# Optimization experiments

Measured on AMD Instinct MI355X. Metric: run time of the kernel, lower is better.

Reference implementation:

```python
import jax, jax.numpy as jnp
import numpy as np

N_NODES = 10000
N_EDGES = 320000
HIDDEN = 256
HEADS = 8
HEAD_DIM = HIDDEN // HEADS  # 32
NEG_SLOPE = 0.2


def setup_inputs() -> dict:
    key = jax.random.key(0)
    ks = jax.random.split(key, 12)
    x = jax.random.normal(ks[0], (N_NODES, HIDDEN), dtype=jnp.float32)
    edges_idx = jax.random.randint(ks[1], (2, N_EDGES), 0, N_NODES, dtype=jnp.int64)
    s = 1.0 / np.sqrt(HIDDEN)
    # layer 1 params
    W1 = jax.random.normal(ks[2], (HIDDEN, HEADS * HEAD_DIM), dtype=jnp.float32) * s
    a_src1 = jax.random.normal(ks[3], (HEADS, HEAD_DIM), dtype=jnp.float32) * s
    a_dst1 = jax.random.normal(ks[4], (HEADS, HEAD_DIM), dtype=jnp.float32) * s
    b1 = jnp.zeros((HEADS * HEAD_DIM,), dtype=jnp.float32)
    # layer 2 params
    W2 = jax.random.normal(ks[5], (HIDDEN, HEADS * HEAD_DIM), dtype=jnp.float32) * s
    a_src2 = jax.random.normal(ks[6], (HEADS, HEAD_DIM), dtype=jnp.float32) * s
    a_dst2 = jax.random.normal(ks[7], (HEADS, HEAD_DIM), dtype=jnp.float32) * s
    b2 = jnp.zeros((HEADS * HEAD_DIM,), dtype=jnp.float32)
    return {"x": x, "edges_idx": edges_idx,
            "W1": W1, "a_src1": a_src1, "a_dst1": a_dst1, "b1": b1,
            "W2": W2, "a_src2": a_src2, "a_dst2": a_dst2, "b2": b2}


def gat_conv(x, src, dst, W, a_src, a_dst, b):
    """PyG GATConv (concat=True, negative_slope=0.2), dropout in eval mode."""
    N = x.shape[0]
    h = (x @ W).reshape(N, HEADS, HEAD_DIM)          # [N,H,C]
    alpha_s = jnp.einsum('nhc,hc->nh', h, a_src)     # [N,H]
    alpha_d = jnp.einsum('nhc,hc->nh', h, a_dst)     # [N,H]
    e = alpha_s[src] + alpha_d[dst]                  # [E,H]
    e = jnp.where(e > 0, e, NEG_SLOPE * e)           # leaky_relu
    # scatter-softmax over incoming edges of each dst node
    m = jax.ops.segment_max(e, dst, num_segments=N)  # [N,H]
    ex = jnp.exp(e - m[dst])                         # [E,H]
    denom = jax.ops.segment_sum(ex, dst, num_segments=N)  # [N,H]
    alpha = ex / (denom[dst] + 1e-16)                # [E,H]
    msg = h[src] * alpha[:, :, None]                 # [E,H,C]
    out = jax.ops.segment_sum(msg, dst, num_segments=N)   # [N,H,C]
    return out.reshape(N, HEADS * HEAD_DIM) + b


def reference(x, edges_idx, W1, a_src1, a_dst1, b1, W2, a_src2, a_dst2, b2):
    src = edges_idx[0]
    dst = edges_idx[1]
    h = gat_conv(x, src, dst, W1, a_src1, a_dst1, b1)
    h = jax.nn.elu(h)
    out = gat_conv(h, src, dst, W2, a_src2, a_dst2, b2)
    return out
```

## Files before the change

### kernel.cpp

```cpp
#include <hip/hip_runtime.h>
#include <hip/hip_bf16.h>
#include <hip/hip_fp16.h>

#define N_NODES 10000
#define N_EDGES 320000
#define HIDDEN 256
#define HEADS 8
#define HEAD_DIM 32
#define NEG_SLOPE 0.2f
#define CAP 80

typedef __attribute__((ext_vector_type(8))) short short8;
typedef __attribute__((ext_vector_type(8))) _Float16 half8;
typedef __attribute__((ext_vector_type(4))) float f32x4;

__device__ __forceinline__ void bf16_split(float v, unsigned short& hi, unsigned short& lo) {
    __hip_bfloat16 hb = __float2bfloat16(v);
    float hf = __bfloat162float(hb);
    __hip_bfloat16 lb = __float2bfloat16(v - hf);
    hi = *reinterpret_cast<unsigned short*>(&hb);
    lo = *reinterpret_cast<unsigned short*>(&lb);
}

__global__ __launch_bounds__(256) void prep_kernel(
    const float* __restrict__ W1, const float* __restrict__ W2,
    const int* __restrict__ src, const int* __restrict__ dst,
    unsigned short* __restrict__ w1h, unsigned short* __restrict__ w1l,
    unsigned short* __restrict__ w2h, unsigned short* __restrict__ w2l,
    int* __restrict__ counts, int* __restrict__ csr_src) {
    int b = blockIdx.x;
    int tid = threadIdx.x;
    if (b < 512) {
        int i = b * 256 + tid;
        int which = i >> 16;
        int rem = i & 0xFFFF;
        int k = rem >> 8, n = rem & 255;
        const float* W = which ? W2 : W1;
        unsigned short* wh = which ? w2h : w1h;
        unsigned short* wl = which ? w2l : w1l;
        unsigned short h, l;
        bf16_split(W[k * 256 + n], h, l);
        wh[n * 256 + k] = h;
        wl[n * 256 + k] = l;
    } else {
        int e = (b - 512) * 256 + tid;
        int d = dst[e];
        int rank = atomicAdd(&counts[d], 1);
        csr_src[d * CAP + rank] = src[e];
    }
}

template <int AFP32>
__global__ __launch_bounds__(256) void gemm_mfma_kernel(
    const float* __restrict__ Axf,
    const unsigned short* __restrict__ Ah, const unsigned short* __restrict__ Al,
    const unsigned short* __restrict__ BhT, const unsigned short* __restrict__ BlT,
    _Float16* __restrict__ hH, const float* __restrict__ a_src,
    const float* __restrict__ a_dst, float* __restrict__ alpha_s,
    float* __restrict__ alpha_d) {
    __shared__ __align__(16) unsigned short sAh[80 * 40];
    __shared__ __align__(16) unsigned short sAl[80 * 40];
    __shared__ __align__(16) unsigned short sBh[128 * 40];
    __shared__ __align__(16) unsigned short sBl[128 * 40];
    __shared__ __align__(16) _Float16 sOut[80 * 264];
    const int tid = threadIdx.x;
    const int w = tid >> 6, lane = tid & 63;
    const int col = lane & 15, quad = lane >> 4;
    const int m0 = blockIdx.y * 80, n0 = blockIdx.x * 128;

    f32x4 acc[5][2] = {};

    float4 raf[3];
    uint4 rau[3];
    uint4 rb[4];

#define LOAD_A(k0)                                                              \
    if (AFP32) {                                                                \
        _Pragma("unroll") for (int i = 0; i < 3; ++i) {                         \
            int t = tid + i * 256;                                              \
            if (t < 640) {                                                      \
                int row = t >> 3, seg = t & 7;                                  \
                raf[i] = *(const float4*)&Axf[(size_t)(m0 + row) * 256 + (k0) + seg * 4]; \
            }                                                                   \
        }                                                                       \
    } else {                                                                    \
        _Pragma("unroll") for (int i = 0; i < 3; ++i) {                         \
            int t = tid + i * 256;                                              \
            if (t < 640) {                                                      \
                int tt = t < 320 ? t : t - 320;                                 \
                int row = tt >> 2, seg = tt & 3;                                \
                const unsigned short* P = t < 320 ? Ah : Al;                    \
                rau[i] = *(const uint4*)&P[(size_t)(m0 + row) * 256 + (k0) + seg * 8]; \
            }                                                                   \
        }                                                                       \
    }
#define LOAD_B(k0)                                                              \
    _Pragma("unroll") for (int i = 0; i < 4; ++i) {                             \
        int t = tid + i * 256;                                                  \
        int tt = t < 512 ? t : t - 512;                                         \
        int row = tt >> 2, seg = tt & 3;                                        \
        const unsigned short* P = t < 512 ? BhT : BlT;                          \
        rb[i] = *(const uint4*)&P[(size_t)(n0 + row) * 256 + (k0) + seg * 8];   \
    }

    LOAD_A(0)
    LOAD_B(0)

    for (int ks = 0; ks < 8; ++ks) {
        if (AFP32) {
#pragma unroll
            for (int i = 0; i < 3; ++i) {
                int t = tid + i * 256;
                if (t < 640) {
                    int row = t >> 3, seg = t & 7;
                    float4 v = raf[i];
                    ushort4 hh, ll;
                    unsigned short hb, lb;
                    bf16_split(v.x, hb, lb); hh.x = hb; ll.x = lb;
                    bf16_split(v.y, hb, lb); hh.y = hb; ll.y = lb;
                    bf16_split(v.z, hb, lb); hh.z = hb; ll.z = lb;
                    bf16_split(v.w, hb, lb); hh.w = hb; ll.w = lb;
                    *(ushort4*)&sAh[row * 40 + seg * 4] = hh;
                    *(ushort4*)&sAl[row * 40 + seg * 4] = ll;
                }
            }
        } else {
#pragma unroll
            for (int i = 0; i < 3; ++i) {
                int t = tid + i * 256;
                if (t < 640) {
                    int tt = t < 320 ? t : t - 320;
                    int row = tt >> 2, seg = tt & 3;
                    unsigned short* S = t < 320 ? sAh : sAl;
                    *(uint4*)&S[row * 40 + seg * 8] = rau[i];
                }
            }
        }
#pragma unroll
        for (int i = 0; i < 4; ++i) {
            int t = tid + i * 256;
            int tt = t < 512 ? t : t - 512;
            int row = tt >> 2, seg = tt & 3;
            unsigned short* S = t < 512 ? sBh : sBl;
            *(uint4*)&S[row * 40 + seg * 8] = rb[i];
        }
        __syncthreads();

        if (ks < 7) {
            int nk = (ks + 1) * 32;
            LOAD_A(nk)
            LOAD_B(nk)
        }

        short8 bh0 = *(const short8*)&sBh[(w * 32 + col) * 40 + quad * 8];
        short8 bl0 = *(const short8*)&sBl[(w * 32 + col) * 40 + quad * 8];
        short8 bh1 = *(const short8*)&sBh[(w * 32 + 16 + col) * 40 + quad * 8];
        short8 bl1 = *(const short8*)&sBl[(w * 32 + 16 + col) * 40 + quad * 8];
#pragma unroll
        for (int rt = 0; rt < 5; ++rt) {
            short8 ah = *(const short8*)&sAh[(rt * 16 + col) * 40 + quad * 8];
            short8 al = *(const short8*)&sAl[(rt * 16 + col) * 40 + quad * 8];
            acc[rt][0] = __builtin_amdgcn_mfma_f32_16x16x32_bf16(ah, bh0, acc[rt][0], 0, 0, 0);
            acc[rt][0] = __builtin_amdgcn_mfma_f32_16x16x32_bf16(ah, bl0, acc[rt][0], 0, 0, 0);
            acc[rt][0] = __builtin_amdgcn_mfma_f32_16x16x32_bf16(al, bh0, acc[rt][0], 0, 0, 0);
            acc[rt][1] = __builtin_amdgcn_mfma_f32_16x16x32_bf16(ah, bh1, acc[rt][1], 0, 0, 0);
            acc[rt][1] = __builtin_amdgcn_mfma_f32_16x16x32_bf16(ah, bl1, acc[rt][1], 0, 0, 0);
            acc[rt][1] = __builtin_amdgcn_mfma_f32_16x16x32_bf16(al, bh1, acc[rt][1], 0, 0, 0);
        }
        __syncthreads();
    }
#undef LOAD_A
#undef LOAD_B

    const int head = blockIdx.x * 4 + w;
    float as0 = a_src[n0 + w * 32 + col];
    float as1 = a_src[n0 + w * 32 + 16 + col];
    float ad0 = a_dst[n0 + w * 32 + col];
    float ad1 = a_dst[n0 + w * 32 + 16 + col];
#pragma unroll
    for (int rt = 0; rt < 5; ++rt) {
#pragma unroll
        for (int r = 0; r < 4; ++r) {
            int row = rt * 16 + quad * 4 + r;
            sOut[row * 264 + w * 32 + col]      = (_Float16)acc[rt][0][r];
            sOut[row * 264 + w * 32 + 16 + col] = (_Float16)acc[rt][1][r];
            float ps = acc[rt][0][r] * as0 + acc[rt][1][r] * as1;
            float pd = acc[rt][0][r] * ad0 + acc[rt][1][r] * ad1;
#pragma unroll
            for (int m = 1; m < 16; m <<= 1) {
                ps += __shfl_xor(ps, m);
                pd += __shfl_xor(pd, m);
            }
            if (col == 0) {
                int gm = m0 + row;
                alpha_s[gm * HEADS + head] = ps;
                alpha_d[gm * HEADS + head] = pd;
            }
        }
    }
    __syncthreads();
#pragma unroll
    for (int i = 0; i < 5; ++i) {
        int t = tid + i * 256;
        int row = t >> 4, seg = t & 15;
        *(half8*)&hH[(size_t)(m0 + row) * 256 + n0 + seg * 8] =
            *(const half8*)&sOut[row * 264 + seg * 8];
    }
}

__global__ __launch_bounds__(256) void aggregate_kernel(
    const int* __restrict__ counts, const int* __restrict__ csr_src,
    const float* __restrict__ alpha_s, const float* __restrict__ alpha_d,
    const _Float16* __restrict__ hH, const float* __restrict__ bias,
    float* __restrict__ outf, unsigned short* __restrict__ oh,
    unsigned short* __restrict__ ol, int mode) {
    const int tid = threadIdx.x;
    const int w = tid >> 6, lane = tid & 63;
    const int ph = blockIdx.x / 2500;
    const int d = (blockIdx.x - ph * 2500) * 4 + w;
    const int q = lane >> 4, fl = lane & 15;
    const int hd = ph * 4 + (fl >> 2);
    const float ad = alpha_d[d * HEADS + hd];
    const int n = counts[d];
    const int* __restrict__ bucket = csr_src + d * CAP;

    const _Float16* hp = hH + ph * 128 + fl * 8;
    float acc[8] = {};
    float den = 0.f;

    int i = q * 4;
    for (; i + 3 < n; i += 16) {
        int4 s4 = *(const int4*)&bucket[i];
        float al0 = alpha_s[s4.x * HEADS + hd];
        float al1 = alpha_s[s4.y * HEADS + hd];
        float al2 = alpha_s[s4.z * HEADS + hd];
        float al3 = alpha_s[s4.w * HEADS + hd];
        half8 h0 = *(const half8*)&hp[(size_t)s4.x * HIDDEN];
        half8 h1 = *(const half8*)&hp[(size_t)s4.y * HIDDEN];
        half8 h2 = *(const half8*)&hp[(size_t)s4.z * HIDDEN];
        half8 h3 = *(const half8*)&hp[(size_t)s4.w * HIDDEN];
        float e0 = al0 + ad; e0 = e0 > 0.f ? e0 : NEG_SLOPE * e0;
        float e1 = al1 + ad; e1 = e1 > 0.f ? e1 : NEG_SLOPE * e1;
        float e2 = al2 + ad; e2 = e2 > 0.f ? e2 : NEG_SLOPE * e2;
        float e3 = al3 + ad; e3 = e3 > 0.f ? e3 : NEG_SLOPE * e3;
        float ev0 = __expf(e0), ev1 = __expf(e1);
        float ev2 = __expf(e2), ev3 = __expf(e3);
        den += (ev0 + ev1) + (ev2 + ev3);
#pragma unroll
        for (int j = 0; j < 8; ++j)
            acc[j] += (float)h0[j] * ev0 + (float)h1[j] * ev1 +
                      (float)h2[j] * ev2 + (float)h3[j] * ev3;
    }
    for (; i < n; ++i) {
        int s0 = bucket[i];
        float al0 = alpha_s[s0 * HEADS + hd];
        half8 h0 = *(const half8*)&hp[(size_t)s0 * HIDDEN];
        float e0 = al0 + ad; e0 = e0 > 0.f ? e0 : NEG_SLOPE * e0;
        float ev0 = __expf(e0);
        den += ev0;
#pragma unroll
        for (int j = 0; j < 8; ++j) acc[j] += (float)h0[j] * ev0;
    }

#pragma unroll
    for (int j = 0; j < 8; ++j) acc[j] += __shfl_xor(acc[j], 16);
    den += __shfl_xor(den, 16);
#pragma unroll
    for (int j = 0; j < 8; ++j) acc[j] += __shfl_xor(acc[j], 32);
    den += __shfl_xor(den, 32);

    if (q == 0) {
        float inv = 1.f / (den + 1e-16f);
        float v[8];
#pragma unroll
        for (int j = 0; j < 8; ++j)
            v[j] = acc[j] * inv + bias[ph * 128 + fl * 8 + j];
        size_t oidx = (size_t)d * HIDDEN + ph * 128 + fl * 8;
        if (mode == 1) {
            unsigned short hb[8], lb[8];
#pragma unroll
            for (int j = 0; j < 8; ++j) {
                v[j] = v[j] > 0.f ? v[j] : (__expf(v[j]) - 1.f);
                bf16_split(v[j], hb[j], lb[j]);
            }
            *(ushort4*)&oh[oidx]     = make_ushort4(hb[0], hb[1], hb[2], hb[3]);
            *(ushort4*)&oh[oidx + 4] = make_ushort4(hb[4], hb[5], hb[6], hb[7]);
            *(ushort4*)&ol[oidx]     = make_ushort4(lb[0], lb[1], lb[2], lb[3]);
            *(ushort4*)&ol[oidx + 4] = make_ushort4(lb[4], lb[5], lb[6], lb[7]);
        } else {
            *(float4*)&outf[oidx]     = make_float4(v[0], v[1], v[2], v[3]);
            *(float4*)&outf[oidx + 4] = make_float4(v[4], v[5], v[6], v[7]);
        }
    }
}

extern "C" void kernel_launch(void* const* d_in, const int* in_sizes, int n_in,
                              void* d_out, int out_size, void* d_ws, size_t ws_size,
                              hipStream_t stream) {
    const float* x      = (const float*)d_in[0];
    const int*   edges  = (const int*)d_in[1];
    const float* W1     = (const float*)d_in[2];
    const float* as1    = (const float*)d_in[3];
    const float* ad1    = (const float*)d_in[4];
    const float* b1     = (const float*)d_in[5];
    const float* W2     = (const float*)d_in[6];
    const float* as2    = (const float*)d_in[7];
    const float* ad2    = (const float*)d_in[8];
    const float* b2     = (const float*)d_in[9];
    float* out = (float*)d_out;

    const int* src = edges;
    const int* dst = edges + N_EDGES;

    const size_t NF = (size_t)N_NODES * HIDDEN;
    const size_t NH = (size_t)N_NODES * HEADS;

    char* base = (char*)d_ws;
    _Float16* hH = (_Float16*)base;             base += NF * 2;
    unsigned short* x2h = (unsigned short*)base; base += NF * 2;
    unsigned short* x2l = (unsigned short*)base; base += NF * 2;
    float* alpha_s = (float*)base;              base += NH * 4;
    float* alpha_d = (float*)base;              base += NH * 4;
    unsigned short* w1h = (unsigned short*)base; base += 65536 * 2;
    unsigned short* w1l = (unsigned short*)base; base += 65536 * 2;
    unsigned short* w2h = (unsigned short*)base; base += 65536 * 2;
    unsigned short* w2l = (unsigned short*)base; base += 65536 * 2;
    int* csr_src = (int*)base;                  base += (size_t)N_NODES * CAP * 4;
    int* counts  = (int*)base;                  base += (size_t)N_NODES * 4;

    dim3 gemm_grid(2, 125);
    const int EB = (N_EDGES + 255) / 256;
    const int AGG_B = 2500 * 2;

    hipMemsetAsync(counts, 0, N_NODES * sizeof(int), stream);
    prep_kernel<<<512 + EB, 256, 0, stream>>>(W1, W2, src, dst,
                                              w1h, w1l, w2h, w2l, counts, csr_src);

    gemm_mfma_kernel<1><<<gemm_grid, 256, 0, stream>>>(
        x, nullptr, nullptr, w1h, w1l, hH, as1, ad1, alpha_s, alpha_d);
    aggregate_kernel<<<AGG_B, 256, 0, stream>>>(counts, csr_src, alpha_s, alpha_d,
                                                hH, b1, nullptr, x2h, x2l, 1);

    gemm_mfma_kernel<0><<<gemm_grid, 256, 0, stream>>>(
        nullptr, x2h, x2l, w2h, w2l, hH, as2, ad2, alpha_s, alpha_d);
    aggregate_kernel<<<AGG_B, 256, 0, stream>>>(counts, csr_src, alpha_s, alpha_d,
                                                hH, b2, out, nullptr, nullptr, 0);
}
```

Baseline: 195.6 us.

## Double-buffer GEMM register prefetch and software-pipeline aggregate gathers

The GEMM kernel now holds two register stages of A/B tiles, so global loads are issued two k-steps ahead of their use rather than one. The aggregate kernel drops the variable-trip loop for a fully unrolled sequence of up to five 16-edge chunks, each with clamped indices and masked exponents, so the next chunk's gathers are issued before the current chunk is computed. Both changes aim to hide global memory latency with more loads in flight. The cost is higher register pressure, which can lower occupancy, and the aggregate path is limited to at most 80 edges per node (CAP).

```diff
diff --git a/kernel.cpp b/kernel.cpp
--- a/kernel.cpp
+++ b/kernel.cpp
@@ -70,17 +70,17 @@
 
     f32x4 acc[5][2] = {};
 
-    float4 raf[3];
-    uint4 rau[3];
-    uint4 rb[4];
-
-#define LOAD_A(k0)                                                              \
+    float4 raf[2][3];
+    uint4 rau[2][3];
+    uint4 rb[2][4];
+
+#define LOAD_A(k0, SS)                                                          \
     if (AFP32) {                                                                \
         _Pragma("unroll") for (int i = 0; i < 3; ++i) {                         \
             int t = tid + i * 256;                                              \
             if (t < 640) {                                                      \
                 int row = t >> 3, seg = t & 7;                                  \
-                raf[i] = *(const float4*)&Axf[(size_t)(m0 + row) * 256 + (k0) + seg * 4]; \
+                raf[SS][i] = *(const float4*)&Axf[(size_t)(m0 + row) * 256 + (k0) + seg * 4]; \
             }                                                                   \
         }                                                                       \
     } else {                                                                    \
@@ -90,66 +90,69 @@
                 int tt = t < 320 ? t : t - 320;                                 \
                 int row = tt >> 2, seg = tt & 3;                                \
                 const unsigned short* P = t < 320 ? Ah : Al;                    \
-                rau[i] = *(const uint4*)&P[(size_t)(m0 + row) * 256 + (k0) + seg * 8]; \
+                rau[SS][i] = *(const uint4*)&P[(size_t)(m0 + row) * 256 + (k0) + seg * 8]; \
             }                                                                   \
         }                                                                       \
     }
-#define LOAD_B(k0)                                                              \
+#define LOAD_B(k0, SS)                                                          \
     _Pragma("unroll") for (int i = 0; i < 4; ++i) {                             \
         int t = tid + i * 256;                                                  \
         int tt = t < 512 ? t : t - 512;                                         \
         int row = tt >> 2, seg = tt & 3;                                        \
         const unsigned short* P = t < 512 ? BhT : BlT;                          \
-        rb[i] = *(const uint4*)&P[(size_t)(n0 + row) * 256 + (k0) + seg * 8];   \
-    }
-
-    LOAD_A(0)
-    LOAD_B(0)
-
+        rb[SS][i] = *(const uint4*)&P[(size_t)(n0 + row) * 256 + (k0) + seg * 8]; \
+    }
+#define WRITE_A(SS)                                                             \
+    if (AFP32) {                                                                \
+        _Pragma("unroll") for (int i = 0; i < 3; ++i) {                         \
+            int t = tid + i * 256;                                              \
+            if (t < 640) {                                                      \
+                int row = t >> 3, seg = t & 7;                                  \
+                float4 v = raf[SS][i];                                          \
+                ushort4 hh, ll;                                                 \
+                unsigned short hb, lb;                                          \
+                bf16_split(v.x, hb, lb); hh.x = hb; ll.x = lb;                  \
+                bf16_split(v.y, hb, lb); hh.y = hb; ll.y = lb;                  \
+                bf16_split(v.z, hb, lb); hh.z = hb; ll.z = lb;                  \
+                bf16_split(v.w, hb, lb); hh.w = hb; ll.w = lb;                  \
+                *(ushort4*)&sAh[row * 40 + seg * 4] = hh;                       \
+                *(ushort4*)&sAl[row * 40 + seg * 4] = ll;                       \
+            }                                                                   \
+        }                                                                       \
+    } else {                                                                    \
+        _Pragma("unroll") for (int i = 0; i < 3; ++i) {                         \
+            int t = tid + i * 256;                                              \
+            if (t < 640) {                                                      \
+                int tt = t < 320 ? t : t - 320;                                 \
+                int row = tt >> 2, seg = tt & 3;                                \
+                unsigned short* Sp = t < 320 ? sAh : sAl;                       \
+                *(uint4*)&Sp[row * 40 + seg * 8] = rau[SS][i];                  \
+            }                                                                   \
+        }                                                                       \
+    }
+#define WRITE_B(SS)                                                             \
+    _Pragma("unroll") for (int i = 0; i < 4; ++i) {                             \
+        int t = tid + i * 256;                                                  \
+        int tt = t < 512 ? t : t - 512;                                         \
+        int row = tt >> 2, seg = tt & 3;                                        \
+        unsigned short* Sp = t < 512 ? sBh : sBl;                               \
+        *(uint4*)&Sp[row * 40 + seg * 8] = rb[SS][i];                           \
+    }
+
+    LOAD_A(0, 0)
+    LOAD_B(0, 0)
+    LOAD_A(32, 1)
+    LOAD_B(32, 1)
+
+#pragma unroll
     for (int ks = 0; ks < 8; ++ks) {
-        if (AFP32) {
-#pragma unroll
-            for (int i = 0; i < 3; ++i) {
-                int t = tid + i * 256;
-                if (t < 640) {
-                    int row = t >> 3, seg = t & 7;
-                    float4 v = raf[i];
-                    ushort4 hh, ll;
-                    unsigned short hb, lb;
-                    bf16_split(v.x, hb, lb); hh.x = hb; ll.x = lb;
-                    bf16_split(v.y, hb, lb); hh.y = hb; ll.y = lb;
-                    bf16_split(v.z, hb, lb); hh.z = hb; ll.z = lb;
-                    bf16_split(v.w, hb, lb); hh.w = hb; ll.w = lb;
-                    *(ushort4*)&sAh[row * 40 + seg * 4] = hh;
-                    *(ushort4*)&sAl[row * 40 + seg * 4] = ll;
-                }
-            }
-        } else {
-#pragma unroll
-            for (int i = 0; i < 3; ++i) {
-                int t = tid + i * 256;
-                if (t < 640) {
-                    int tt = t < 320 ? t : t - 320;
-                    int row = tt >> 2, seg = tt & 3;
-                    unsigned short* S = t < 320 ? sAh : sAl;
-                    *(uint4*)&S[row * 40 + seg * 8] = rau[i];
-                }
-            }
-        }
-#pragma unroll
-        for (int i = 0; i < 4; ++i) {
-            int t = tid + i * 256;
-            int tt = t < 512 ? t : t - 512;
-            int row = tt >> 2, seg = tt & 3;
-            unsigned short* S = t < 512 ? sBh : sBl;
-            *(uint4*)&S[row * 40 + seg * 8] = rb[i];
-        }
+        WRITE_A(ks & 1)
+        WRITE_B(ks & 1)
         __syncthreads();
 
-        if (ks < 7) {
-            int nk = (ks + 1) * 32;
-            LOAD_A(nk)
-            LOAD_B(nk)
+        if (ks < 6) {
+            LOAD_A((ks + 2) * 32, ks & 1)
+            LOAD_B((ks + 2) * 32, ks & 1)
         }
 
         short8 bh0 = *(const short8*)&sBh[(w * 32 + col) * 40 + quad * 8];
@@ -171,6 +174,8 @@
     }
 #undef LOAD_A
 #undef LOAD_B
+#undef WRITE_A
+#undef WRITE_B
 
     const int head = blockIdx.x * 4 + w;
     float as0 = a_src[n0 + w * 32 + col];
@@ -223,44 +228,71 @@
     const float ad = alpha_d[d * HEADS + hd];
     const int n = counts[d];
     const int* __restrict__ bucket = csr_src + d * CAP;
+    const int qb = q * 4;
 
     const _Float16* hp = hH + ph * 128 + fl * 8;
     float acc[8] = {};
     float den = 0.f;
 
-    int i = q * 4;
-    for (; i + 3 < n; i += 16) {
-        int4 s4 = *(const int4*)&bucket[i];
-        float al0 = alpha_s[s4.x * HEADS + hd];
-        float al1 = alpha_s[s4.y * HEADS + hd];
-        float al2 = alpha_s[s4.z * HEADS + hd];
-        float al3 = alpha_s[s4.w * HEADS + hd];
-        half8 h0 = *(const half8*)&hp[(size_t)s4.x * HIDDEN];
-        half8 h1 = *(const half8*)&hp[(size_t)s4.y * HIDDEN];
-        half8 h2 = *(const half8*)&hp[(size_t)s4.z * HIDDEN];
-        half8 h3 = *(const half8*)&hp[(size_t)s4.w * HIDDEN];
-        float e0 = al0 + ad; e0 = e0 > 0.f ? e0 : NEG_SLOPE * e0;
-        float e1 = al1 + ad; e1 = e1 > 0.f ? e1 : NEG_SLOPE * e1;
-        float e2 = al2 + ad; e2 = e2 > 0.f ? e2 : NEG_SLOPE * e2;
-        float e3 = al3 + ad; e3 = e3 > 0.f ? e3 : NEG_SLOPE * e3;
-        float ev0 = __expf(e0), ev1 = __expf(e1);
-        float ev2 = __expf(e2), ev3 = __expf(e3);
-        den += (ev0 + ev1) + (ev2 + ev3);
-#pragma unroll
-        for (int j = 0; j < 8; ++j)
-            acc[j] += (float)h0[j] * ev0 + (float)h1[j] * ev1 +
-                      (float)h2[j] * ev2 + (float)h3[j] * ev3;
-    }
-    for (; i < n; ++i) {
-        int s0 = bucket[i];
-        float al0 = alpha_s[s0 * HEADS + hd];
-        half8 h0 = *(const half8*)&hp[(size_t)s0 * HIDDEN];
-        float e0 = al0 + ad; e0 = e0 > 0.f ? e0 : NEG_SLOPE * e0;
-        float ev0 = __expf(e0);
-        den += ev0;
-#pragma unroll
-        for (int j = 0; j < 8; ++j) acc[j] += (float)h0[j] * ev0;
-    }
+    int4 s0_ = make_int4(0, 0, 0, 0), s1_ = s0_, s2_ = s0_, s3_ = s0_, s4_ = s0_;
+    if (n > 0)  s0_ = *(const int4*)&bucket[qb];
+    if (n > 16) s1_ = *(const int4*)&bucket[qb + 16];
+    if (n > 32) s2_ = *(const int4*)&bucket[qb + 32];
+    if (n > 48) s3_ = *(const int4*)&bucket[qb + 48];
+    if (n > 64) s4_ = *(const int4*)&bucket[qb + 64];
+
+#define AGG_DECL(t) float al##t##0, al##t##1, al##t##2, al##t##3;               \
+                    half8 hv##t##0, hv##t##1, hv##t##2, hv##t##3;
+    AGG_DECL(0) AGG_DECL(1) AGG_DECL(2) AGG_DECL(3) AGG_DECL(4)
+
+#define AGG_CLAMP(x) ((x) < 0 ? 0 : ((x) > 9999 ? 9999 : (x)))
+#define AGG_GATHER(t, sv)                                                       \
+    {                                                                           \
+        int i0_ = AGG_CLAMP((sv).x), i1_ = AGG_CLAMP((sv).y);                   \
+        int i2_ = AGG_CLAMP((sv).z), i3_ = AGG_CLAMP((sv).w);                   \
+        al##t##0 = alpha_s[i0_ * HEADS + hd];                                   \
+        al##t##1 = alpha_s[i1_ * HEADS + hd];                                   \
+        al##t##2 = alpha_s[i2_ * HEADS + hd];                                   \
+        al##t##3 = alpha_s[i3_ * HEADS + hd];                                   \
+        hv##t##0 = *(const half8*)&hp[(size_t)i0_ * HIDDEN];                    \
+        hv##t##1 = *(const half8*)&hp[(size_t)i1_ * HIDDEN];                    \
+        hv##t##2 = *(const half8*)&hp[(size_t)i2_ * HIDDEN];                    \
+        hv##t##3 = *(const half8*)&hp[(size_t)i3_ * HIDDEN];                    \
+    }
+#define AGG_COMPUTE(t, base)                                                    \
+    {                                                                           \
+        int b0_ = (base) + qb;                                                  \
+        float e0 = al##t##0 + ad; e0 = e0 > 0.f ? e0 : NEG_SLOPE * e0;          \
+        float e1 = al##t##1 + ad; e1 = e1 > 0.f ? e1 : NEG_SLOPE * e1;          \
+        float e2 = al##t##2 + ad; e2 = e2 > 0.f ? e2 : NEG_SLOPE * e2;          \
+        float e3 = al##t##3 + ad; e3 = e3 > 0.f ? e3 : NEG_SLOPE * e3;          \
+        if (b0_ >= n)     e0 = -1e30f;                                          \
+        if (b0_ + 1 >= n) e1 = -1e30f;                                          \
+        if (b0_ + 2 >= n) e2 = -1e30f;                                          \
+        if (b0_ + 3 >= n) e3 = -1e30f;                                          \
+        float ev0 = __expf(e0), ev1 = __expf(e1);                               \
+        float ev2 = __expf(e2), ev3 = __expf(e3);                               \
+        den += (ev0 + ev1) + (ev2 + ev3);                                       \
+        _Pragma("unroll") for (int j = 0; j < 8; ++j)                           \
+            acc[j] += (float)hv##t##0[j] * ev0 + (float)hv##t##1[j] * ev1 +     \
+                      (float)hv##t##2[j] * ev2 + (float)hv##t##3[j] * ev3;      \
+    }
+
+    if (n > 0)  AGG_GATHER(0, s0_)
+    if (n > 16) AGG_GATHER(1, s1_)
+    if (n > 0)  AGG_COMPUTE(0, 0)
+    if (n > 32) AGG_GATHER(2, s2_)
+    if (n > 16) AGG_COMPUTE(1, 16)
+    if (n > 48) AGG_GATHER(3, s3_)
+    if (n > 32) AGG_COMPUTE(2, 32)
+    if (n > 64) AGG_GATHER(4, s4_)
+    if (n > 48) AGG_COMPUTE(3, 48)
+    if (n > 64) AGG_COMPUTE(4, 64)
+
+#undef AGG_DECL
+#undef AGG_CLAMP
+#undef AGG_GATHER
+#undef AGG_COMPUTE
 
 #pragma unroll
     for (int j = 0; j < 8; ++j) acc[j] += __shfl_xor(acc[j], 16);
```

Measured after the change: 198.3 us. No clear change (+1.4%).
